# Kernel tuning notes

Hardware: AMD Instinct MI355X
Metric: run time of the kernel (lower is better)

## Reference

```python
import jax, jax.numpy as jnp
import numpy as np

B, C, H, W = 8, 64, 256, 256
V = H * W
E = (H - 1) * W + H * (W - 1)  # vertical + horizontal grid edges
N_ROUNDS = int(np.ceil(np.log2(V)))  # Boruvka halves #components per round


def build_index():
    # matches _build_matrix_index: raw_index[y, x] = y * W + x
    raw = jnp.arange(V, dtype=jnp.int32).reshape(H, W)
    row_e = jnp.stack([raw[:-1, :], raw[1:, :]], axis=-1).reshape(-1, 2)  # vertical edges
    col_e = jnp.stack([raw[:, :-1], raw[:, 1:]], axis=-1).reshape(-1, 2)  # horizontal edges
    return jnp.concatenate([row_e, col_e], axis=0)  # [E, 2]


def edge_weights(fm):
    # distance_func = squared L2 over channel dim; weight = dist + 1 (so weight >= 1)
    b = fm.shape[0]
    d_row = ((fm[:, :, :-1, :] - fm[:, :, 1:, :]) ** 2).sum(1).reshape(b, -1)
    d_col = ((fm[:, :, :, :-1] - fm[:, :, :, 1:]) ** 2).sum(1).reshape(b, -1)
    return jnp.concatenate([d_row, d_col], axis=1) + 1.0  # [B, E]


def mst_boruvka(u, v, w):
    """Parallel Boruvka MST on a connected graph. u, v: [E] int32, w: [E] float32.
    Returns boolean selection mask over edges (exactly V-1 True)."""
    eidx = jnp.arange(E, dtype=jnp.int32)
    vidx = jnp.arange(V, dtype=jnp.int32)
    INF = jnp.float32(jnp.inf)
    BIG = jnp.int32(E)  # sentinel edge id

    def round_fn(state, _):
        comp, sel = state
        cu, cv = comp[u], comp[v]
        active = cu != cv
        wa = jnp.where(active, w, INF)
        # min outgoing edge weight per component
        minw = jnp.full((V,), INF, jnp.float32).at[cu].min(wa).at[cv].min(wa)
        # tie-break by smallest edge index (consistent tie-break -> no long cycles)
        cand_u = jnp.where(active & (wa == minw[cu]), eidx, BIG)
        cand_v = jnp.where(active & (wa == minw[cv]), eidx, BIG)
        best = jnp.full((V,), BIG, jnp.int32).at[cu].min(cand_u).at[cv].min(cand_v)
        has = best < BIG
        be = jnp.clip(best, 0, E - 1)
        cu_b, cv_b = comp[u[be]], comp[v[be]]
        # hook each component onto the component at the other end of its best edge
        parent = jnp.where(has, jnp.where(cu_b == vidx, cv_b, cu_b), vidx)
        # break mutual 2-cycles: keep the smaller label as root
        pp = parent[parent]
        parent = jnp.where((pp == vidx) & (vidx < parent), vidx, parent)
        # pointer jumping to full path compression
        for _ in range(N_ROUNDS):
            parent = parent[parent]
        comp = parent[comp]
        sel = sel.at[jnp.where(has, best, BIG)].set(True, mode='drop')
        return (comp, sel), None

    init = (vidx, jnp.zeros((E,), dtype=bool))
    (comp, sel), _ = jax.lax.scan(round_fn, init, None, length=N_ROUNDS)
    return sel


def setup_inputs() -> dict:
    key = jax.random.key(0)
    guide_in = jax.random.normal(key, (B, C, H, W), dtype=jnp.float32)
    return {"guide_in": guide_in}


def reference(guide_in):
    index = build_index()                      # [E, 2] shared across batch
    weight = edge_weights(guide_in)            # [B, E]
    u, v = index[:, 0], index[:, 1]
    sel = jax.vmap(lambda wb: mst_boruvka(u, v, wb))(weight)  # [B, E] bool
    # grid graph is connected -> exactly V-1 MST edges per image (static shape)
    eids = jax.vmap(lambda s: jnp.nonzero(s, size=V - 1, fill_value=0)[0])(sel)
    tree = index[eids]                         # [B, V-1, 2] vertex pairs of the MST
    return tree
```

## Files before the change

kernel.cpp:

```cpp
#include <hip/hip_runtime.h>
#include <stdint.h>

typedef unsigned long long ull;

#define Bc 8
#define Cc 64
#define Hc 256
#define Wc 256
#define Vc (Hc*Wc)
#define REc ((Hc-1)*Wc)
#define Ec (REc + Hc*(Wc-1))
#define VM1 (Vc-1)
#define INF64 0xFFFFFFFFFFFFFFFFull
#define NRND 16
#define EPB 8192
#define BPB 16

__device__ __forceinline__ void edge_uv(int e, int& u, int& v){
  if (e < REc){ u = e; v = e + Wc; }
  else { int k = e - REc; int i = k / (Wc-1); int j = k - i*(Wc-1); u = i*Wc + j; v = u + 1; }
}

__device__ __forceinline__ ull packw(float w, int e){
  return ((ull)__float_as_uint(w) << 32) | (unsigned)e;
}

__device__ __forceinline__ int chase(const int* __restrict__ parB, int x){
  int p = parB[x];
  while (p != x){ x = p; p = parB[x]; }
  return x;
}

__global__ void __launch_bounds__(1024)
k_weights(const float* __restrict__ g, float* __restrict__ wf,
          int* __restrict__ L, int* __restrict__ par,
          ull* __restrict__ b0, ull* __restrict__ b1,
          unsigned char* __restrict__ sel, int* __restrict__ act, int* __restrict__ outp){
  int t = blockIdx.x*1024 + threadIdx.x;
  int b = t >> 16; int v = t & VM1;
  int i = v >> 8, j = v & (Wc-1);
  const bool hU = i > 0, hD = i < Hc-1, hL = j > 0, hR = j < Wc-1;
  const int oU = hU ? -Wc : 0, oD = hD ? Wc : 0, oL = hL ? -1 : 0, oR = hR ? 1 : 0;
  const float* p = g + (size_t)b*Cc*Vc + v;
  float sU = 0.f, sD = 0.f, sL = 0.f, sR = 0.f;
  #pragma unroll 4
  for (int c = 0; c < Cc; ++c){
    const float* pc = p + (size_t)c*Vc;
    float x = pc[0];
    float dU = x - pc[oU];  float dD = x - pc[oD];
    float dL = x - pc[oL];  float dR = x - pc[oR];
    sU += dU*dU; sD += dD*dD; sL += dL*dL; sR += dR*dR;
  }
  float wU = sU + 1.0f, wD = sD + 1.0f, wL = sL + 1.0f, wR = sR + 1.0f;
  int eU = v - Wc, eD = v, eL = REc + i*(Wc-1) + j - 1, eR = REc + i*(Wc-1) + j;
  ull m = INF64;
  if (hU){ ull x = packw(wU, eU); if (x < m) m = x; }
  if (hD){ ull x = packw(wD, eD); if (x < m) m = x; }
  if (hL){ ull x = packw(wL, eL); if (x < m) m = x; }
  if (hR){ ull x = packw(wR, eR); if (x < m) m = x; }
  b0[t] = m;
  b1[t] = INF64;
  L[t] = v; par[t] = v;
  float* wfb = wf + (size_t)b*Ec;
  unsigned char* selb = sel + (size_t)b*Ec;
  if (hD){ wfb[eD] = wD; selb[eD] = 0; }
  if (hR){ wfb[eR] = wR; selb[eR] = 0; }
  if (t < Bc*VM1){ outp[2*t] = 0; outp[2*t+1] = Wc; }
  if (t < (NRND+2)*Bc) act[t] = 0;
}

__global__ void __launch_bounds__(1024)
k_scanmerge(const float* __restrict__ wf, int* __restrict__ L,
            const int* __restrict__ par,
            ull* __restrict__ bcur, ull* __restrict__ bnxt,
            const int* __restrict__ act, int r){
  int t = blockIdx.x*1024 + threadIdx.x;
  int b = t >> 16;
  if (!act[r*Bc + b]) return;
  int v = t & VM1; const int base = b << 16;
  const int* parB = par + base;
  int Lt0 = L[t];
  int i = v >> 8, j = v & (Wc-1);
  int Lu = (i > 0)    ? L[base + v - Wc] : Lt0;
  int Ld = (i < Hc-1) ? L[base + v + Wc] : Lt0;
  int Ll = (j > 0)    ? L[base + v - 1 ] : Lt0;
  int Lr = (j < Wc-1) ? L[base + v + 1 ] : Lt0;
  if ((Lu==Lt0) & (Ld==Lt0) & (Ll==Lt0) & (Lr==Lt0)){
    if (Lt0 != v) return;
    if (parB[v] == v){ bnxt[t] = INF64; return; }
  }
  int rt = chase(parB, Lt0);
  if (rt != Lt0) L[t] = rt;
  if (v == rt) bnxt[t] = INF64;
  const float* wfb = wf + (size_t)b*Ec;
  ull m = INF64;
  if (Lu != Lt0 && Lu != rt && chase(parB, Lu) != rt){
    int e = v - Wc; ull x = packw(wfb[e], e); if (x < m) m = x; }
  if (Ld != Lt0 && Ld != rt && chase(parB, Ld) != rt){
    int e = v;      ull x = packw(wfb[e], e); if (x < m) m = x; }
  if (Ll != Lt0 && Ll != rt && chase(parB, Ll) != rt){
    int e = REc + i*(Wc-1) + j - 1; ull x = packw(wfb[e], e); if (x < m) m = x; }
  if (Lr != Lt0 && Lr != rt && chase(parB, Lr) != rt){
    int e = REc + i*(Wc-1) + j;     ull x = packw(wfb[e], e); if (x < m) m = x; }
  if (m != INF64) atomicMin(&bcur[base + rt], m);
}

__global__ void __launch_bounds__(1024)
k_hook(const int* __restrict__ L, const ull* __restrict__ bcur,
       int* __restrict__ par, unsigned char* __restrict__ sel, int* __restrict__ act, int r){
  int t = blockIdx.x*1024 + threadIdx.x;
  int b = t >> 16;
  if (r > 0 && !act[r*Bc + b]) return;
  int v = t & VM1;
  if (L[t] != v) return;
  const int base = b << 16;
  ull p = bcur[t];
  int pr = v;
  if (p != INF64){
    int e = (int)(unsigned)p; int eu, ev; edge_uv(e, eu, ev);
    int cu = L[base + eu], cv = L[base + ev];
    int other = (cu == v) ? cv : cu;
    sel[(size_t)b*Ec + e] = 1;
    if (act[(r+1)*Bc + b] == 0) act[(r+1)*Bc + b] = 1;
    pr = (bcur[base + other] == p && v < other) ? v : other;
  }
  par[t] = pr;
}

__global__ void __launch_bounds__(1024)
k_cnt(const unsigned char* __restrict__ sel, int* __restrict__ blkcnt){
  int blk = blockIdx.x; int bb = blk / BPB; int kb = blk % BPB;
  int base = kb*EPB;
  int off = threadIdx.x * 8;
  int c = 0;
  if (base + off < Ec){
    const unsigned int* p = (const unsigned int*)(sel + (size_t)bb*Ec + base + off);
    unsigned int s = p[0] + p[1];
    c = (s & 0xFF) + ((s>>8)&0xFF) + ((s>>16)&0xFF) + (s>>24);
  }
  int lane = threadIdx.x & 63, wave = threadIdx.x >> 6;
  #pragma unroll
  for (int o = 32; o; o >>= 1) c += __shfl_down(c, o, 64);
  __shared__ int sw[16];
  if (lane == 0) sw[wave] = c;
  __syncthreads();
  if (threadIdx.x == 0){
    int s = 0;
    #pragma unroll
    for (int w = 0; w < 16; ++w) s += sw[w];
    blkcnt[blk] = s;
  }
}

__global__ void __launch_bounds__(1024)
k_scatter(const unsigned char* __restrict__ sel, const int* __restrict__ blkcnt,
          int* __restrict__ outp){
  int blk = blockIdx.x; int bb = blk / BPB; int kb = blk % BPB;
  __shared__ int s_boff;
  if (threadIdx.x < 64){
    int c = ((int)threadIdx.x < kb) ? blkcnt[bb*BPB + threadIdx.x] : 0;
    #pragma unroll
    for (int o = 32; o; o >>= 1) c += __shfl_down(c, o, 64);
    if (threadIdx.x == 0) s_boff = c;
  }
  int base = kb*EPB;
  int off = threadIdx.x * 8;
  unsigned int a = 0, d = 0; int c = 0;
  if (base + off < Ec){
    const unsigned int* p = (const unsigned int*)(sel + (size_t)bb*Ec + base + off);
    a = p[0]; d = p[1];
    unsigned int s = a + d;
    c = (s & 0xFF) + ((s>>8)&0xFF) + ((s>>16)&0xFF) + (s>>24);
  }
  int lane = threadIdx.x & 63, wave = threadIdx.x >> 6;
  int x = c;
  #pragma unroll
  for (int o = 1; o < 64; o <<= 1){ int y = __shfl_up(x, o, 64); if (lane >= o) x += y; }
  __shared__ int sw[16];
  if (lane == 63) sw[wave] = x;
  __syncthreads();
  int woff = 0;
  #pragma unroll
  for (int w = 0; w < 16; ++w) if (w < wave) woff += sw[w];
  int pos = s_boff + woff + x - c;
  if (base + off < Ec){
    int* ob = outp + (size_t)bb*VM1*2;
    int ebase = base + off;
    #pragma unroll
    for (int k = 0; k < 8; ++k){
      unsigned int byte = ((k < 4) ? (a >> (8*k)) : (d >> (8*(k-4)))) & 0xFF;
      if (byte){ int e = ebase + k; int u, v; edge_uv(e, u, v); ob[2*pos] = u; ob[2*pos+1] = v; ++pos; }
    }
  }
}

extern "C" void kernel_launch(void* const* d_in, const int* in_sizes, int n_in,
                              void* d_out, int out_size, void* d_ws, size_t ws_size,
                              hipStream_t stream) {
  const float* g = (const float*)d_in[0];
  int* outp = (int*)d_out;

  char* ws = (char*)d_ws;
  size_t off = 0;
  auto alloc = [&](size_t bytes) -> void* {
    void* p = ws + off; off += (bytes + 511) & ~(size_t)511; return p;
  };
  ull* b0 = (ull*)alloc((size_t)Bc*Vc*8);
  ull* b1 = (ull*)alloc((size_t)Bc*Vc*8);
  float* wf = (float*)alloc((size_t)Bc*Ec*4);
  int* L   = (int*)alloc((size_t)Bc*Vc*4);
  int* par = (int*)alloc((size_t)Bc*Vc*4);
  unsigned char* sel = (unsigned char*)alloc((size_t)Bc*Ec);
  int* act  = (int*)alloc((size_t)(NRND+2)*Bc*4);
  int* blkcnt = (int*)alloc((size_t)Bc*BPB*4);

  const int gv = (Bc*Vc)/1024;

  k_weights<<<gv, 1024, 0, stream>>>(g, wf, L, par, b0, b1, sel, act, outp);
  k_hook   <<<gv, 1024, 0, stream>>>(L, b0, par, sel, act, 0);
  for (int r = 1; r < NRND; ++r){
    ull* bcur = (r & 1) ? b1 : b0;
    ull* bnxt = (r & 1) ? b0 : b1;
    k_scanmerge<<<gv, 1024, 0, stream>>>(wf, L, par, bcur, bnxt, act, r);
    k_hook     <<<gv, 1024, 0, stream>>>(L, bcur, par, sel, act, r);
  }
  k_cnt    <<<Bc*BPB, 1024, 0, stream>>>(sel, blkcnt);
  k_scatter<<<Bc*BPB, 1024, 0, stream>>>(sel, blkcnt, outp);
}
```

Baseline: 248.3 us.

## Run Boruvka locally per 32x32 tile in shared memory, then finish on contracted edge list

Replaces the 31 global-memory Boruvka launches with two stages. The first computes weights and runs Boruvka inside each 32x32 tile in LDS, restricted to edges whose endpoints both lie in the tile, then compacts the remaining cross-component edges into a list. The second runs one block per image with 128KB of shared labels and contracts over the shrinking edge list for up to 20 rounds. This removes many launches and much global traffic. The risk is that the finish stage uses only 8 blocks, so it may be serial and latency-bound, and tile-local MST decisions must stay consistent with the global tie-breaking order.

```diff
diff --git a/kernel.cpp b/kernel.cpp
--- a/kernel.cpp
+++ b/kernel.cpp
@@ -2,6 +2,8 @@
 #include <stdint.h>
 
 typedef unsigned long long ull;
+typedef unsigned short u16;
+typedef unsigned int u32;
 
 #define Bc 8
 #define Cc 64
@@ -12,7 +14,8 @@
 #define Ec (REc + Hc*(Wc-1))
 #define VM1 (Vc-1)
 #define INF64 0xFFFFFFFFFFFFFFFFull
-#define NRND 16
+#define TS 32
+#define MAXF 20
 #define EPB 8192
 #define BPB 16
 
@@ -25,106 +28,194 @@
   return ((ull)__float_as_uint(w) << 32) | (unsigned)e;
 }
 
-__device__ __forceinline__ int chase(const int* __restrict__ parB, int x){
-  int p = parB[x];
-  while (p != x){ x = p; p = parB[x]; }
-  return x;
-}
-
 __global__ void __launch_bounds__(1024)
-k_weights(const float* __restrict__ g, float* __restrict__ wf,
-          int* __restrict__ L, int* __restrict__ par,
-          ull* __restrict__ b0, ull* __restrict__ b1,
-          unsigned char* __restrict__ sel, int* __restrict__ act, int* __restrict__ outp){
-  int t = blockIdx.x*1024 + threadIdx.x;
-  int b = t >> 16; int v = t & VM1;
-  int i = v >> 8, j = v & (Wc-1);
+k_stage1(const float* __restrict__ g, float* __restrict__ wf,
+         u16* __restrict__ L16, unsigned char* __restrict__ sel,
+         int* __restrict__ elist, int* __restrict__ ecnt, int* __restrict__ outp){
+  const int blk = blockIdx.x;
+  const int b = blk >> 6, tile = blk & 63;
+  const int ty = tile >> 3, tx = tile & 7;
+  const int tid = threadIdx.x;
+  const int li = tid >> 5, lj = tid & 31;
+  const int i = ty*TS + li, j = tx*TS + lj;
+  const int v = (i << 8) | j;
+
   const bool hU = i > 0, hD = i < Hc-1, hL = j > 0, hR = j < Wc-1;
   const int oU = hU ? -Wc : 0, oD = hD ? Wc : 0, oL = hL ? -1 : 0, oR = hR ? 1 : 0;
   const float* p = g + (size_t)b*Cc*Vc + v;
-  float sU = 0.f, sD = 0.f, sL = 0.f, sR = 0.f;
+  float sU=0.f, sD=0.f, sL=0.f, sR=0.f;
   #pragma unroll 4
   for (int c = 0; c < Cc; ++c){
     const float* pc = p + (size_t)c*Vc;
     float x = pc[0];
-    float dU = x - pc[oU];  float dD = x - pc[oD];
-    float dL = x - pc[oL];  float dR = x - pc[oR];
+    float dU = x - pc[oU]; float dD = x - pc[oD];
+    float dL = x - pc[oL]; float dR = x - pc[oR];
     sU += dU*dU; sD += dD*dD; sL += dL*dL; sR += dR*dR;
   }
-  float wU = sU + 1.0f, wD = sD + 1.0f, wL = sL + 1.0f, wR = sR + 1.0f;
-  int eU = v - Wc, eD = v, eL = REc + i*(Wc-1) + j - 1, eR = REc + i*(Wc-1) + j;
-  ull m = INF64;
-  if (hU){ ull x = packw(wU, eU); if (x < m) m = x; }
-  if (hD){ ull x = packw(wD, eD); if (x < m) m = x; }
-  if (hL){ ull x = packw(wL, eL); if (x < m) m = x; }
-  if (hR){ ull x = packw(wR, eR); if (x < m) m = x; }
-  b0[t] = m;
-  b1[t] = INF64;
-  L[t] = v; par[t] = v;
+  const int eU = v - Wc, eD = v, eL = REc + i*(Wc-1) + j - 1, eR = REc + i*(Wc-1) + j;
+  const ull pU = packw(sU+1.f, eU), pD = packw(sD+1.f, eD);
+  const ull pL = packw(sL+1.f, eL), pR = packw(sR+1.f, eR);
   float* wfb = wf + (size_t)b*Ec;
   unsigned char* selb = sel + (size_t)b*Ec;
-  if (hD){ wfb[eD] = wD; selb[eD] = 0; }
-  if (hR){ wfb[eR] = wR; selb[eR] = 0; }
-  if (t < Bc*VM1){ outp[2*t] = 0; outp[2*t+1] = Wc; }
-  if (t < (NRND+2)*Bc) act[t] = 0;
-}
-
-__global__ void __launch_bounds__(1024)
-k_scanmerge(const float* __restrict__ wf, int* __restrict__ L,
-            const int* __restrict__ par,
-            ull* __restrict__ bcur, ull* __restrict__ bnxt,
-            const int* __restrict__ act, int r){
-  int t = blockIdx.x*1024 + threadIdx.x;
-  int b = t >> 16;
-  if (!act[r*Bc + b]) return;
-  int v = t & VM1; const int base = b << 16;
-  const int* parB = par + base;
-  int Lt0 = L[t];
-  int i = v >> 8, j = v & (Wc-1);
-  int Lu = (i > 0)    ? L[base + v - Wc] : Lt0;
-  int Ld = (i < Hc-1) ? L[base + v + Wc] : Lt0;
-  int Ll = (j > 0)    ? L[base + v - 1 ] : Lt0;
-  int Lr = (j < Wc-1) ? L[base + v + 1 ] : Lt0;
-  if ((Lu==Lt0) & (Ld==Lt0) & (Ll==Lt0) & (Lr==Lt0)){
-    if (Lt0 != v) return;
-    if (parB[v] == v){ bnxt[t] = INF64; return; }
-  }
-  int rt = chase(parB, Lt0);
-  if (rt != Lt0) L[t] = rt;
-  if (v == rt) bnxt[t] = INF64;
+  if (hD){ wfb[eD] = sD+1.f; selb[eD] = 0; }
+  if (hR){ wfb[eR] = sR+1.f; selb[eR] = 0; }
+  { int gt = blk*1024 + tid; if (gt < Bc*VM1){ outp[2*gt] = 0; outp[2*gt+1] = Wc; } }
+
+  __shared__ u16 lab[1024];
+  __shared__ u16 spar[1024];
+  __shared__ ull best[1024];
+  __shared__ int s_any;
+  lab[tid] = (u16)tid;
+
+  for (int round = 0; round < 16; ++round){
+    best[tid] = INF64;
+    if (tid == 0) s_any = 0;
+    __syncthreads();
+    int c = lab[tid];
+    ull m = INF64;
+    if (hU){ bool inc = (li > 0)    ? (lab[tid-TS] != c) : true; if (inc && pU < m) m = pU; }
+    if (hD){ bool inc = (li < TS-1) ? (lab[tid+TS] != c) : true; if (inc && pD < m) m = pD; }
+    if (hL){ bool inc = (lj > 0)    ? (lab[tid-1 ] != c) : true; if (inc && pL < m) m = pL; }
+    if (hR){ bool inc = (lj < TS-1) ? (lab[tid+1 ] != c) : true; if (inc && pR < m) m = pR; }
+    if (m != INF64) atomicMin(&best[c], m);
+    __syncthreads();
+    int pr = tid;
+    if (c == tid){
+      ull pb = best[tid];
+      if (pb != INF64){
+        int e = (int)(unsigned)pb; int eu, ev; edge_uv(e, eu, ev);
+        int diu = (eu>>8) - ty*TS, dju = (eu&255) - tx*TS;
+        int div_ = (ev>>8) - ty*TS, djv = (ev&255) - tx*TS;
+        bool inu  = ((unsigned)diu < TS) && ((unsigned)dju < TS);
+        bool inv_ = ((unsigned)div_ < TS) && ((unsigned)djv < TS);
+        if (inu && inv_){
+          int lu = diu*TS + dju, lv = div_*TS + djv;
+          int cu = lab[lu], cv = lab[lv];
+          int other = (cu == tid) ? cv : cu;
+          sel[(size_t)b*Ec + e] = 1;
+          s_any = 1;
+          pr = (best[other] == pb && tid < other) ? tid : other;
+        }
+      }
+    }
+    spar[tid] = (u16)pr;
+    __syncthreads();
+    int x = lab[tid];
+    int pp = spar[x];
+    while (pp != x){ x = pp; pp = spar[x]; }
+    int any = s_any;
+    lab[tid] = (u16)x;
+    __syncthreads();
+    if (!any) break;
+  }
+
+  int rt = lab[tid];
+  int groot = ((ty*TS + (rt>>5)) << 8) | (tx*TS + (rt&31));
+  L16[((size_t)b<<16) + v] = (u16)groot;
+
+  int e1 = -1, e2 = -1, cnt = 0;
+  if (hD){ bool a_ = (li < TS-1) ? (lab[tid] != lab[tid+TS]) : true; if (a_){ e1 = eD; ++cnt; } }
+  if (hR){ bool a_ = (lj < TS-1) ? (lab[tid] != lab[tid+1 ]) : true; if (a_){ e2 = eR; ++cnt; } }
+  int lane = tid & 63, wave = tid >> 6;
+  int xs = cnt;
+  #pragma unroll
+  for (int o = 1; o < 64; o <<= 1){ int y = __shfl_up(xs, o, 64); if (lane >= o) xs += y; }
+  __shared__ int sw[16];
+  __shared__ int s_base;
+  if (lane == 63) sw[wave] = xs;
+  __syncthreads();
+  if (tid == 0){
+    int tot = 0;
+    #pragma unroll
+    for (int w = 0; w < 16; ++w){ int t_ = sw[w]; sw[w] = tot; tot += t_; }
+    s_base = atomicAdd(&ecnt[b], tot);
+  }
+  __syncthreads();
+  int pos = s_base + sw[wave] + xs - cnt;
+  int* el = elist + (size_t)b*Ec;
+  if (e1 >= 0) el[pos++] = e1;
+  if (e2 >= 0) el[pos]   = e2;
+}
+
+__global__ void __launch_bounds__(1024,1)
+k_finish(const float* __restrict__ wf, const u16* __restrict__ L16,
+         ull* __restrict__ bestA, int* __restrict__ parA,
+         unsigned char* __restrict__ sel, int* __restrict__ elA, int* __restrict__ elB,
+         const int* __restrict__ ecnt){
+  extern __shared__ u16 lab[];
+  __shared__ int sw[16];
+  __shared__ int s_tot;
+  const int b = blockIdx.x;
+  const int tid = threadIdx.x;
+  const size_t base = (size_t)b << 16;
+  const u32* ls = (const u32*)(L16 + base);
+  u32* ld = (u32*)lab;
+  for (int k = tid; k < Vc/2; k += 1024) ld[k] = ls[k];
+  ull* best = bestA + base;
+  int* par  = parA + base;
   const float* wfb = wf + (size_t)b*Ec;
-  ull m = INF64;
-  if (Lu != Lt0 && Lu != rt && chase(parB, Lu) != rt){
-    int e = v - Wc; ull x = packw(wfb[e], e); if (x < m) m = x; }
-  if (Ld != Lt0 && Ld != rt && chase(parB, Ld) != rt){
-    int e = v;      ull x = packw(wfb[e], e); if (x < m) m = x; }
-  if (Ll != Lt0 && Ll != rt && chase(parB, Ll) != rt){
-    int e = REc + i*(Wc-1) + j - 1; ull x = packw(wfb[e], e); if (x < m) m = x; }
-  if (Lr != Lt0 && Lr != rt && chase(parB, Lr) != rt){
-    int e = REc + i*(Wc-1) + j;     ull x = packw(wfb[e], e); if (x < m) m = x; }
-  if (m != INF64) atomicMin(&bcur[base + rt], m);
-}
-
-__global__ void __launch_bounds__(1024)
-k_hook(const int* __restrict__ L, const ull* __restrict__ bcur,
-       int* __restrict__ par, unsigned char* __restrict__ sel, int* __restrict__ act, int r){
-  int t = blockIdx.x*1024 + threadIdx.x;
-  int b = t >> 16;
-  if (r > 0 && !act[r*Bc + b]) return;
-  int v = t & VM1;
-  if (L[t] != v) return;
-  const int base = b << 16;
-  ull p = bcur[t];
-  int pr = v;
-  if (p != INF64){
-    int e = (int)(unsigned)p; int eu, ev; edge_uv(e, eu, ev);
-    int cu = L[base + eu], cv = L[base + ev];
-    int other = (cu == v) ? cv : cu;
-    sel[(size_t)b*Ec + e] = 1;
-    if (act[(r+1)*Bc + b] == 0) act[(r+1)*Bc + b] = 1;
-    pr = (bcur[base + other] == p && v < other) ? v : other;
-  }
-  par[t] = pr;
+  unsigned char* selb = sel + (size_t)b*Ec;
+  int* cur = elA + (size_t)b*Ec;
+  int* nxt = elB + (size_t)b*Ec;
+  int m = ecnt[b];
+  __syncthreads();
+
+  for (int round = 0; round < MAXF && m > 0; ++round){
+    for (int k = tid; k < m; k += 1024){
+      int e = cur[k]; int u, v; edge_uv(e, u, v);
+      int cu = lab[u], cv = lab[v];
+      best[cu] = INF64; best[cv] = INF64; par[cu] = cu; par[cv] = cv;
+    }
+    __syncthreads();
+    for (int k = tid; k < m; k += 1024){
+      int e = cur[k]; int u, v; edge_uv(e, u, v);
+      ull pk = packw(wfb[e], e);
+      atomicMin(&best[lab[u]], pk); atomicMin(&best[lab[v]], pk);
+    }
+    __syncthreads();
+    for (int k = tid; k < m; k += 1024){
+      int e = cur[k]; int u, v; edge_uv(e, u, v);
+      int cu = lab[u], cv = lab[v];
+      ull pk = packw(wfb[e], e);
+      ull bu_ = atomicMin(&best[cu], INF64);
+      ull bv_ = atomicMin(&best[cv], INF64);
+      bool bu = (bu_ == pk), bv = (bv_ == pk);
+      if (bu | bv) selb[e] = 1;
+      if (bu) par[cu] = (bv && cu < cv) ? cu : cv;
+      if (bv) par[cv] = (bu && cv < cu) ? cv : cu;
+    }
+    __syncthreads();
+    int cnt = 0;
+    for (int k = tid; k < m; k += 1024){
+      int e = cur[k]; int u, v; edge_uv(e, u, v);
+      int ru = lab[u]; { int pp = par[ru]; while (pp != ru){ ru = pp; pp = par[ru]; } }
+      int rv = lab[v]; { int pp = par[rv]; while (pp != rv){ rv = pp; pp = par[rv]; } }
+      lab[u] = (u16)ru; lab[v] = (u16)rv;
+      if (ru != rv) ++cnt;
+    }
+    __syncthreads();
+    int lane = tid & 63, wave = tid >> 6;
+    int xs = cnt;
+    #pragma unroll
+    for (int o = 1; o < 64; o <<= 1){ int y = __shfl_up(xs, o, 64); if (lane >= o) xs += y; }
+    if (lane == 63) sw[wave] = xs;
+    __syncthreads();
+    if (tid == 0){
+      int tot = 0;
+      #pragma unroll
+      for (int w = 0; w < 16; ++w){ int t_ = sw[w]; sw[w] = tot; tot += t_; }
+      s_tot = tot;
+    }
+    __syncthreads();
+    int pos = sw[wave] + xs - cnt;
+    for (int k = tid; k < m; k += 1024){
+      int e = cur[k]; int u, v; edge_uv(e, u, v);
+      if (lab[u] != lab[v]) nxt[pos++] = e;
+    }
+    m = s_tot;
+    int* t_ = cur; cur = nxt; nxt = t_;
+    __syncthreads();
+  }
 }
 
 __global__ void __launch_bounds__(1024)
@@ -205,25 +296,19 @@
   auto alloc = [&](size_t bytes) -> void* {
     void* p = ws + off; off += (bytes + 511) & ~(size_t)511; return p;
   };
-  ull* b0 = (ull*)alloc((size_t)Bc*Vc*8);
-  ull* b1 = (ull*)alloc((size_t)Bc*Vc*8);
+  ull* best = (ull*)alloc((size_t)Bc*Vc*8);
   float* wf = (float*)alloc((size_t)Bc*Ec*4);
-  int* L   = (int*)alloc((size_t)Bc*Vc*4);
-  int* par = (int*)alloc((size_t)Bc*Vc*4);
+  int* par  = (int*)alloc((size_t)Bc*Vc*4);
+  u16* L16  = (u16*)alloc((size_t)Bc*Vc*2);
   unsigned char* sel = (unsigned char*)alloc((size_t)Bc*Ec);
-  int* act  = (int*)alloc((size_t)(NRND+2)*Bc*4);
+  int* elA  = (int*)alloc((size_t)Bc*Ec*4);
+  int* elB  = (int*)alloc((size_t)Bc*Ec*4);
+  int* ecnt = (int*)alloc((size_t)Bc*4);
   int* blkcnt = (int*)alloc((size_t)Bc*BPB*4);
 
-  const int gv = (Bc*Vc)/1024;
-
-  k_weights<<<gv, 1024, 0, stream>>>(g, wf, L, par, b0, b1, sel, act, outp);
-  k_hook   <<<gv, 1024, 0, stream>>>(L, b0, par, sel, act, 0);
-  for (int r = 1; r < NRND; ++r){
-    ull* bcur = (r & 1) ? b1 : b0;
-    ull* bnxt = (r & 1) ? b0 : b1;
-    k_scanmerge<<<gv, 1024, 0, stream>>>(wf, L, par, bcur, bnxt, act, r);
-    k_hook     <<<gv, 1024, 0, stream>>>(L, bcur, par, sel, act, r);
-  }
+  hipMemsetAsync(ecnt, 0, (size_t)Bc*4, stream);
+  k_stage1<<<Bc*64, 1024, 0, stream>>>(g, wf, L16, sel, elA, ecnt, outp);
+  k_finish<<<Bc, 1024, 131072, stream>>>(wf, L16, best, par, sel, elA, elB, ecnt);
   k_cnt    <<<Bc*BPB, 1024, 0, stream>>>(sel, blkcnt);
   k_scatter<<<Bc*BPB, 1024, 0, stream>>>(sel, blkcnt, outp);
 }
```

New measurement: 809.8 us. 3.26x slower.
